# Optimization experiments

Hardware: AMD Instinct MI355X
Metric: run time of the kernel (lower is better)

## Reference

```python
import jax, jax.numpy as jnp
import numpy as np

B = 32; L = 512; D_MODEL = 512; N_LAYERS = 4
D_STATE = 64; D_CONV = 4; EXPAND = 2; HEADDIM = 64; PRED = 96
D_INNER = EXPAND * D_MODEL            # 1024
NHEADS = D_INNER // HEADDIM           # 16
CONV_DIM = D_INNER + 2 * D_STATE      # 1152
D_IN_PROJ = 2 * D_INNER + 2 * D_STATE + NHEADS  # 2192
EPS = 1e-5


def setup_inputs() -> dict:
    key = jax.random.key(0)
    ks = jax.random.split(key, 8)
    s = lambda k, shape, scale=0.02: jax.random.normal(k, shape, jnp.float32) * scale
    return {
        "x": jax.random.normal(ks[0], (B, L, D_MODEL), jnp.float32),
        "in_proj_w": s(ks[1], (N_LAYERS, D_IN_PROJ, D_MODEL)),
        "conv_w": s(ks[2], (N_LAYERS, CONV_DIM, D_CONV), 0.2),
        "conv_b": jnp.zeros((N_LAYERS, CONV_DIM), jnp.float32),
        "dt_bias": jnp.log(jnp.expm1(jax.random.uniform(ks[3], (N_LAYERS, NHEADS), minval=0.001, maxval=0.1))),
        "A_log": jnp.log(jax.random.uniform(ks[4], (N_LAYERS, NHEADS), minval=1.0, maxval=16.0)),
        "Dp": jnp.ones((N_LAYERS, NHEADS), jnp.float32),
        "norm_w": jnp.ones((N_LAYERS, D_INNER), jnp.float32),
        "out_proj_w": s(ks[5], (N_LAYERS, D_MODEL, D_INNER)),
        "ln_w": jnp.ones((N_LAYERS, D_MODEL), jnp.float32),
        "ln_b": jnp.zeros((N_LAYERS, D_MODEL), jnp.float32),
        "final_w": s(ks[6], (D_MODEL, D_MODEL)),
        "final_b": jnp.zeros((D_MODEL,), jnp.float32),
    }


def _silu(x):
    return x * jax.nn.sigmoid(x)


def _causal_dwconv(x, w, b):
    # x: (B, L, C); depthwise causal conv, kernel D_CONV, left pad D_CONV-1
    xt = jnp.swapaxes(x, 1, 2)  # (B, C, L)
    y = jax.lax.conv_general_dilated(
        xt, w[:, None, :], window_strides=(1,), padding=[(D_CONV - 1, 0)],
        feature_group_count=CONV_DIM, dimension_numbers=("NCH", "OIH", "NCH"))
    return jnp.swapaxes(y + b[None, :, None], 1, 2)


def _ssd_scan(xh, dt, Bm, Cm, A, Dp):
    # xh: (B,L,H,P), dt: (B,L,H), Bm/Cm: (B,L,N), A/Dp: (H,)
    dA = jnp.exp(dt * A)  # (B,L,H)

    def step(h, t):
        dA_t, x_t, dt_t, B_t, C_t = t  # (B,H), (B,H,P), (B,H), (B,N), (B,N)
        h = h * dA_t[:, :, None, None] + (dt_t[:, :, None] * x_t)[..., None] * B_t[:, None, None, :]
        y = jnp.einsum("bhpn,bn->bhp", h, C_t)
        return h, y

    Bb, Ll, H, P = xh.shape
    N = Bm.shape[-1]
    h0 = jnp.zeros((Bb, H, P, N), xh.dtype)
    xs = (jnp.moveaxis(dA, 1, 0), jnp.moveaxis(xh, 1, 0), jnp.moveaxis(dt, 1, 0),
          jnp.moveaxis(Bm, 1, 0), jnp.moveaxis(Cm, 1, 0))
    _, ys = jax.lax.scan(step, h0, xs)
    y = jnp.moveaxis(ys, 0, 1)  # (B,L,H,P)
    return y + xh * Dp[None, None, :, None]


def _mamba2(x, w_in, cw, cb, dtb, a_log, dp, nw, w_out):
    zxbcdt = jnp.einsum("bld,ed->ble", x, w_in)  # (B,L,D_IN_PROJ)
    z = zxbcdt[..., :D_INNER]
    xBC = zxbcdt[..., D_INNER:D_INNER + CONV_DIM]
    dt = jax.nn.softplus(zxbcdt[..., -NHEADS:] + dtb)
    xBC = _silu(_causal_dwconv(xBC, cw, cb))
    xh = xBC[..., :D_INNER].reshape(x.shape[0], x.shape[1], NHEADS, HEADDIM)
    Bm = xBC[..., D_INNER:D_INNER + D_STATE]
    Cm = xBC[..., D_INNER + D_STATE:]
    A = -jnp.exp(a_log)
    y = _ssd_scan(xh, dt, Bm, Cm, A, dp).reshape(x.shape[0], x.shape[1], D_INNER)
    # gated RMSNorm (norm_before_gate=False): gate first, then normalize
    y = y * _silu(z)
    y = y * jax.lax.rsqrt(jnp.mean(y * y, axis=-1, keepdims=True) + EPS) * nw
    return jnp.einsum("ble,de->bld", y, w_out)


def _layernorm(x, w, b):
    xc = x - jnp.mean(x, axis=-1, keepdims=True)
    return xc * jax.lax.rsqrt(jnp.mean(xc * xc, axis=-1, keepdims=True) + EPS) * w + b


def reference(x, in_proj_w, conv_w, conv_b, dt_bias, A_log, Dp, norm_w,
              out_proj_w, ln_w, ln_b, final_w, final_b):
    h = x
    for i in range(N_LAYERS):
        res = h
        h = _mamba2(h, in_proj_w[i], conv_w[i], conv_b[i], dt_bias[i],
                    A_log[i], Dp[i], norm_w[i], out_proj_w[i])
        h = _layernorm(h + res, ln_w[i], ln_b[i])
        # dropout is identity in eval mode
    h = h[:, -PRED:, :]
    return jnp.einsum("bld,ed->ble", h, final_w) + final_b
```

## Files before the change

kernel.cpp:

```cpp
#include <hip/hip_runtime.h>
#include <stdint.h>

#define BATCH 32
#define SEQ   512
#define DM    512
#define NL    4
#define DSTATE 64
#define DI    1024
#define NH    16
#define HD    64
#define PREDN 96
#define CDIM  1152
#define CSEG  144
#define DPROJ 2192
#define XBW   1168
#define NC    8
#define EPSF  1e-5f

typedef float  f32x4  __attribute__((ext_vector_type(4)));
typedef __bf16 bf16x4 __attribute__((ext_vector_type(4)));
typedef __bf16 bf16x8 __attribute__((ext_vector_type(8)));

__device__ __forceinline__ float sigmoidf_(float x){ return 1.f/(1.f+__expf(-x)); }
__device__ __forceinline__ float siluf_(float x){ return x*sigmoidf_(x); }
__device__ __forceinline__ float softplusf_(float x){ return (x>20.f)?x:log1pf(__expf(x)); }

__device__ __forceinline__ void gld16(const void* g, void* l){
  __builtin_amdgcn_global_load_lds((__attribute__((address_space(1))) void*)g,
                                   (__attribute__((address_space(3))) void*)l, 16, 0, 0);
}

template<typename TC>
__global__ __launch_bounds__(256) void gemm128(
    const __bf16* __restrict__ A, const __bf16* __restrict__ W,
    TC* __restrict__ C, TC* __restrict__ C2, const float* __restrict__ bias,
    int M, int Nreal, int ldc, int ldc2, int splitN, int K, int remapA)
{
  __shared__ __bf16 sAB[2*128*64];
  __bf16* sA = sAB;
  __bf16* sW = sAB + 128*64;
  const int tid  = threadIdx.x;
  const int m0   = blockIdx.y*128, n0 = blockIdx.x*128;
  const int lane = tid&63, wave = tid>>6;
  const int l15  = lane&15, quad = lane>>4;
  const int wr   = (wave>>1)*64, wc = (wave&1)*64;
  f32x4 acc[4][4];
  #pragma unroll
  for (int a=0;a<4;++a)
    #pragma unroll
    for (int b=0;b<4;++b) acc[a][b] = (f32x4){0,0,0,0};

  for (int k0=0; k0<K; k0+=64){
    #pragma unroll
    for (int j=0;j<4;++j){
      const int f = j*256 + tid;
      const int r = f>>3;
      const int kc = (((f&7) ^ (r&7)))*8;
      int ga = m0 + r;
      if (remapA){ int bb = ga/PREDN; ga = bb*SEQ + (SEQ-PREDN) + (ga - bb*PREDN); }
      gld16(A + (size_t)ga*K + k0 + kc, &sA[f*8]);
      int rb = n0 + r; rb = rb < Nreal ? rb : (Nreal-1);
      gld16(W + (size_t)rb*K + k0 + kc, &sW[f*8]);
    }
    __syncthreads();
    #pragma unroll
    for (int kk=0; kk<64; kk+=32){
      const int kcb = (kk>>3) + quad;
      bf16x8 av[4], bv[4];
      #pragma unroll
      for (int mi=0;mi<4;++mi){
        const int row = wr+mi*16+l15;
        av[mi] = *(const bf16x8*)&sA[row*64 + ((kcb ^ (row&7))<<3)];
      }
      #pragma unroll
      for (int ni=0;ni<4;++ni){
        const int row = wc+ni*16+l15;
        bv[ni] = *(const bf16x8*)&sW[row*64 + ((kcb ^ (row&7))<<3)];
      }
      #pragma unroll
      for (int mi=0;mi<4;++mi)
        #pragma unroll
        for (int ni=0;ni<4;++ni)
          acc[mi][ni] = __builtin_amdgcn_mfma_f32_16x16x32_bf16(av[mi],bv[ni],acc[mi][ni],0,0,0);
    }
    __syncthreads();
  }

  if constexpr (sizeof(TC)==2){
    #pragma unroll
    for (int mi=0;mi<4;++mi)
      #pragma unroll
      for (int ni=0;ni<4;++ni)
        #pragma unroll
        for (int r4=0;r4<4;++r4){
          const int row = wr+mi*16+quad*4+r4;
          const int col = wc+ni*16+l15;
          const int g2  = (col>>3) ^ (row&15);
          sAB[row*128 + g2*8 + (col&7)] = (__bf16)acc[mi][ni][r4];
        }
    __syncthreads();
    #pragma unroll
    for (int it=0; it<8; ++it){
      const int idx = it*256 + tid;
      const int row = idx>>4, g = idx&15;
      const int g2 = g ^ (row&15);
      bf16x8 v = *(const bf16x8*)&sAB[row*128 + g2*8];
      const int col0 = n0 + g*8;
      if (col0 < Nreal){
        const int grow = m0 + row;
        if (col0 < splitN) *(bf16x8*)&C [(size_t)grow*ldc  + col0]          = v;
        else               *(bf16x8*)&C2[(size_t)grow*ldc2 + (col0-splitN)] = v;
      }
    }
  } else {
    #pragma unroll
    for (int ni=0;ni<4;++ni){
      const int col = n0 + wc + ni*16 + l15;
      if (col < Nreal){
        const float badd = bias ? bias[col] : 0.f;
        #pragma unroll
        for (int mi=0;mi<4;++mi){
          #pragma unroll
          for (int r4=0;r4<4;++r4){
            const int row = m0 + wr + mi*16 + quad*4 + r4;
            C[(size_t)row*ldc + col] = (TC)(acc[mi][ni][r4] + badd);
          }
        }
      }
    }
  }
}

__global__ __launch_bounds__(256) void cast4_k(
    const float* __restrict__ s0, __bf16* __restrict__ d0, int n0,
    const float* __restrict__ s1, __bf16* __restrict__ d1, int n1,
    const float* __restrict__ s2, __bf16* __restrict__ d2, int n2,
    const float* __restrict__ s3, __bf16* __restrict__ d3, int n3)
{
  int i = blockIdx.x*256 + threadIdx.x;
  const float* s; __bf16* d;
  if (i < n0){ s=s0; d=d0; }
  else if ((i-=n0) < n1){ s=s1; d=d1; }
  else if ((i-=n1) < n2){ s=s2; d=d2; }
  else if ((i-=n2) < n3){ s=s3; d=d3; }
  else return;
  float4 v = ((const float4*)s)[i];
  bf16x4 o;
  o[0]=(__bf16)v.x; o[1]=(__bf16)v.y; o[2]=(__bf16)v.z; o[3]=(__bf16)v.w;
  ((bf16x4*)d)[i] = o;
}

__global__ __launch_bounds__(256) void conv_silu_k(
    const __bf16* __restrict__ xbw, const float* __restrict__ cw,
    const float* __restrict__ cb, __bf16* __restrict__ xout,
    __bf16* __restrict__ bcout)
{
  int idx = blockIdx.x*256 + threadIdx.x;
  if (idx >= BATCH*SEQ*CSEG) return;
  const int seg = idx % CSEG;
  const int bt  = idx / CSEG;
  const int t = bt % SEQ, b = bt / SEQ;
  const int d0 = seg*8;
  const __bf16* src = xbw + ((size_t)b*SEQ + t)*XBW + d0;
  bf16x8 z8;
  #pragma unroll
  for (int e=0;e<8;++e) z8[e]=(__bf16)0.f;
  bf16x8 x3 = *(const bf16x8*)src;
  bf16x8 x2 = (t>=1)? *(const bf16x8*)(src -   XBW) : z8;
  bf16x8 x1 = (t>=2)? *(const bf16x8*)(src - 2*XBW) : z8;
  bf16x8 x0 = (t>=3)? *(const bf16x8*)(src - 3*XBW) : z8;
  const float4* w4  = (const float4*)(cw + (size_t)d0*4);
  const float4* cb4 = (const float4*)(cb + d0);
  float4 cbl = cb4[0], cbh = cb4[1];
  bf16x8 o;
  #pragma unroll
  for (int e=0;e<8;++e){
    float4 w = w4[e];
    float acc = (e<4 ? (&cbl.x)[e] : (&cbh.x)[e-4])
              + w.x*(float)x0[e] + w.y*(float)x1[e]
              + w.z*(float)x2[e] + w.w*(float)x3[e];
    o[e] = (__bf16)siluf_(acc);
  }
  if (d0 < DI) *(bf16x8*)(xout  + ((size_t)b*SEQ+t)*DI  + d0)       = o;
  else         *(bf16x8*)(bcout + ((size_t)b*SEQ+t)*128 + (d0-DI))  = o;
}

__global__ __launch_bounds__(256) void ssd_fused_k(
    const __bf16* __restrict__ bc,
    __bf16* __restrict__ xy,
    const __bf16* __restrict__ xbw,
    const float* __restrict__ dtb_, const float* __restrict__ alog_,
    const float* __restrict__ dp_)
{
  __shared__ __bf16 sB[64*72], sC[64*72], sXT[64*72], sBwT[64*72],
                    sS[64*72], sHT[64*72];
  __shared__ float sCS[SEQ], sDT[SEQ];
  const int bid = blockIdx.x;
  const int h = bid & 15, b = bid >> 4;
  const int tid = threadIdx.x, wave = tid>>6, lane = tid&63;
  const int l15 = lane&15, quad = lane>>4;
  const int wm = (wave>>1)*32, wn = (wave&1)*32;

  const float Ah  = -__expf(alog_[h]);
  const float dtb = dtb_[h];
  const float Dh  = dp_[h];

  for (int t = tid; t < SEQ; t += 256){
    float raw = (float)xbw[((size_t)b*SEQ + t)*XBW + CDIM + h];
    float dt = softplusf_(raw + dtb);
    sDT[t] = dt;
    sCS[t] = dt*Ah;
  }
  __syncthreads();
  for (int ch = wave; ch < NC; ch += 4){
    float s = sCS[ch*64 + lane];
    #pragma unroll
    for (int off=1; off<64; off<<=1){
      float v = __shfl_up(s, off);
      if (lane >= off) s += v;
    }
    sCS[ch*64 + lane] = s;
  }
  __syncthreads();

  f32x4 run[2][2];
  #pragma unroll
  for (int a=0;a<2;++a)
    #pragma unroll
    for (int d=0;d<2;++d) run[a][d] = (f32x4){0,0,0,0};

  for (int c = 0; c < NC; ++c){
    const int t0 = c*64;
    {
      const int r = tid>>2, seg = (tid&3)*16;
      const __bf16* row = bc + ((size_t)b*SEQ + t0 + r)*128;
      bf16x8 vb0 = *(const bf16x8*)(row + seg);
      bf16x8 vb1 = *(const bf16x8*)(row + seg + 8);
      bf16x8 vc0 = *(const bf16x8*)(row + 64 + seg);
      bf16x8 vc1 = *(const bf16x8*)(row + 64 + seg + 8);
      *(bf16x8*)&sB[r*72+seg]   = vb0;
      *(bf16x8*)&sB[r*72+seg+8] = vb1;
      *(bf16x8*)&sC[r*72+seg]   = vc0;
      *(bf16x8*)&sC[r*72+seg+8] = vc1;
      const float w = __expf(sCS[t0+63] - sCS[t0+r]) * sDT[t0+r];
      #pragma unroll
      for (int e=0;e<8;++e){
        sBwT[(seg+e)*72 + r]   = (__bf16)(w*(float)vb0[e]);
        sBwT[(seg+8+e)*72 + r] = (__bf16)(w*(float)vb1[e]);
      }
      const __bf16* xrow = xy + ((size_t)b*SEQ + t0 + r)*DI + h*64;
      bf16x8 vx0 = *(const bf16x8*)(xrow + seg);
      bf16x8 vx1 = *(const bf16x8*)(xrow + seg + 8);
      #pragma unroll
      for (int e=0;e<8;++e){
        sXT[(seg+e)*72 + r]   = vx0[e];
        sXT[(seg+8+e)*72 + r] = vx1[e];
      }
    }
    __syncthreads();

    f32x4 aS[2][2];
    #pragma unroll
    for (int a=0;a<2;++a)
      #pragma unroll
      for (int d=0;d<2;++d) aS[a][d] = (f32x4){0,0,0,0};
    #pragma unroll
    for (int kk=0; kk<64; kk+=32){
      const int kf = kk + quad*8;
      bf16x8 a0 = *(const bf16x8*)&sC[(wm+l15)*72+kf];
      bf16x8 a1 = *(const bf16x8*)&sC[(wm+16+l15)*72+kf];
      bf16x8 b0 = *(const bf16x8*)&sB[(wn+l15)*72+kf];
      bf16x8 b1 = *(const bf16x8*)&sB[(wn+16+l15)*72+kf];
      aS[0][0] = __builtin_amdgcn_mfma_f32_16x16x32_bf16(a0,b0,aS[0][0],0,0,0);
      aS[0][1] = __builtin_amdgcn_mfma_f32_16x16x32_bf16(a0,b1,aS[0][1],0,0,0);
      aS[1][0] = __builtin_amdgcn_mfma_f32_16x16x32_bf16(a1,b0,aS[1][0],0,0,0);
      aS[1][1] = __builtin_amdgcn_mfma_f32_16x16x32_bf16(a1,b1,aS[1][1],0,0,0);
    }
    #pragma unroll
    for (int mi=0;mi<2;++mi)
      #pragma unroll
      for (int ni=0;ni<2;++ni)
        #pragma unroll
        for (int r4=0;r4<4;++r4){
          const int i = wm+mi*16+quad*4+r4, j = wn+ni*16+l15;
          float ed = __expf(fminf(sCS[t0+i]-sCS[t0+j], 0.f)) * sDT[t0+j];
          float v = aS[mi][ni][r4]*ed;
          sS[i*72+j] = (__bf16)((j<=i)? v : 0.f);
          sHT[j*72+i] = (__bf16)run[mi][ni][r4];
        }
    __syncthreads();

    f32x4 aY[2][2], aH[2][2], aYi[2][2];
    #pragma unroll
    for (int a=0;a<2;++a)
      #pragma unroll
      for (int d=0;d<2;++d){
        aY[a][d]=(f32x4){0,0,0,0}; aH[a][d]=(f32x4){0,0,0,0};
        aYi[a][d]=(f32x4){0,0,0,0};
      }
    #pragma unroll
    for (int kk=0; kk<64; kk+=32){
      const int kf = kk + quad*8;
      bf16x8 b0 = *(const bf16x8*)&sXT[(wn+l15)*72+kf];
      bf16x8 b1 = *(const bf16x8*)&sXT[(wn+16+l15)*72+kf];
      bf16x8 s0 = *(const bf16x8*)&sS[(wm+l15)*72+kf];
      bf16x8 s1 = *(const bf16x8*)&sS[(wm+16+l15)*72+kf];
      bf16x8 w0 = *(const bf16x8*)&sBwT[(wm+l15)*72+kf];
      bf16x8 w1 = *(const bf16x8*)&sBwT[(wm+16+l15)*72+kf];
      bf16x8 c0 = *(const bf16x8*)&sC[(wm+l15)*72+kf];
      bf16x8 c1 = *(const bf16x8*)&sC[(wm+16+l15)*72+kf];
      bf16x8 h0 = *(const bf16x8*)&sHT[(wn+l15)*72+kf];
      bf16x8 h1 = *(const bf16x8*)&sHT[(wn+16+l15)*72+kf];
      aY[0][0] = __builtin_amdgcn_mfma_f32_16x16x32_bf16(s0,b0,aY[0][0],0,0,0);
      aY[0][1] = __builtin_amdgcn_mfma_f32_16x16x32_bf16(s0,b1,aY[0][1],0,0,0);
      aY[1][0] = __builtin_amdgcn_mfma_f32_16x16x32_bf16(s1,b0,aY[1][0],0,0,0);
      aY[1][1] = __builtin_amdgcn_mfma_f32_16x16x32_bf16(s1,b1,aY[1][1],0,0,0);
      aH[0][0] = __builtin_amdgcn_mfma_f32_16x16x32_bf16(w0,b0,aH[0][0],0,0,0);
      aH[0][1] = __builtin_amdgcn_mfma_f32_16x16x32_bf16(w0,b1,aH[0][1],0,0,0);
      aH[1][0] = __builtin_amdgcn_mfma_f32_16x16x32_bf16(w1,b0,aH[1][0],0,0,0);
      aH[1][1] = __builtin_amdgcn_mfma_f32_16x16x32_bf16(w1,b1,aH[1][1],0,0,0);
      aYi[0][0] = __builtin_amdgcn_mfma_f32_16x16x32_bf16(c0,h0,aYi[0][0],0,0,0);
      aYi[0][1] = __builtin_amdgcn_mfma_f32_16x16x32_bf16(c0,h1,aYi[0][1],0,0,0);
      aYi[1][0] = __builtin_amdgcn_mfma_f32_16x16x32_bf16(c1,h0,aYi[1][0],0,0,0);
      aYi[1][1] = __builtin_amdgcn_mfma_f32_16x16x32_bf16(c1,h1,aYi[1][1],0,0,0);
    }

    const float lam = __expf(sCS[t0+63]);
    #pragma unroll
    for (int mi=0;mi<2;++mi)
      #pragma unroll
      for (int ni=0;ni<2;++ni)
        #pragma unroll
        for (int r4=0;r4<4;++r4){
          const int i = wm+mi*16+quad*4+r4;
          const int p = wn+ni*16+l15;
          const float xval = (float)sXT[p*72 + i];
          const float e2 = __expf(sCS[t0+i]);
          const float yv = aY[mi][ni][r4] + Dh*xval + e2*aYi[mi][ni][r4];
          xy[((size_t)b*SEQ + t0 + i)*DI + h*64 + p] = (__bf16)yv;
          run[mi][ni][r4] = run[mi][ni][r4]*lam + aH[mi][ni][r4];
        }
    __syncthreads();
  }
}

__global__ __launch_bounds__(256) void gate_rms_k(
    __bf16* __restrict__ y, const __bf16* __restrict__ z, const float* __restrict__ nw)
{
  __shared__ float red[4];
  const int tid = threadIdx.x;
  const int sub = tid>>7;
  const int off = (tid&127)*8;
  const size_t row = (size_t)blockIdx.x*2 + sub;
  __bf16* yrow = y + row*DI;
  const __bf16* zrow = z + row*DI;
  bf16x8 yv = *(const bf16x8*)(yrow+off);
  bf16x8 zv = *(const bf16x8*)(zrow+off);
  float u[8]; float ss = 0.f;
  #pragma unroll
  for (int e=0;e<8;++e){
    float uu = (float)yv[e]*siluf_((float)zv[e]);
    u[e]=uu; ss += uu*uu;
  }
  #pragma unroll
  for (int o=32;o;o>>=1) ss += __shfl_xor(ss,o);
  if ((tid&63)==0) red[tid>>6] = ss;
  __syncthreads();
  ss = red[sub*2] + red[sub*2+1];
  const float sc = rsqrtf(ss*(1.f/DI) + EPSF);
  const float4* nw4 = (const float4*)(nw + off);
  float4 n0 = nw4[0], n1 = nw4[1];
  bf16x8 o;
  #pragma unroll
  for (int e=0;e<8;++e)
    o[e] = (__bf16)(u[e]*sc*(e<4 ? (&n0.x)[e] : (&n1.x)[e-4]));
  *(bf16x8*)(yrow+off) = o;
}

__global__ __launch_bounds__(256) void add_ln_k(
    const __bf16* __restrict__ tmp, __bf16* __restrict__ resio,
    const float* __restrict__ w, const float* __restrict__ bb)
{
  const int tid = threadIdx.x, lane = tid&63;
  const size_t row = (size_t)blockIdx.x*4 + (tid>>6);
  const int off = lane*8;
  const __bf16* trow = tmp + row*DM;
  __bf16* rrow = resio + row*DM;
  bf16x8 tv = *(const bf16x8*)(trow+off);
  bf16x8 rv = *(const bf16x8*)(rrow+off);
  float v[8]; float s = 0.f;
  #pragma unroll
  for (int e=0;e<8;++e){ v[e]=(float)tv[e]+(float)rv[e]; s += v[e]; }
  #pragma unroll
  for (int o=32;o;o>>=1) s += __shfl_xor(s,o);
  const float mean = s*(1.f/DM);
  float q = 0.f;
  #pragma unroll
  for (int e=0;e<8;++e){ v[e]-=mean; q += v[e]*v[e]; }
  #pragma unroll
  for (int o=32;o;o>>=1) q += __shfl_xor(q,o);
  const float rstd = rsqrtf(q*(1.f/DM) + EPSF);
  const float4* w4 = (const float4*)(w + off);
  const float4* b4 = (const float4*)(bb + off);
  float4 w0=w4[0], w1=w4[1], b0=b4[0], b1=b4[1];
  bf16x8 o8;
  #pragma unroll
  for (int e=0;e<8;++e){
    float we = e<4 ? (&w0.x)[e] : (&w1.x)[e-4];
    float be = e<4 ? (&b0.x)[e] : (&b1.x)[e-4];
    o8[e] = (__bf16)(v[e]*rstd*we + be);
  }
  *(bf16x8*)(rrow+off) = o8;
}

extern "C" void kernel_launch(void* const* d_in, const int* in_sizes, int n_in,
                              void* d_out, int out_size, void* d_ws, size_t ws_size,
                              hipStream_t stream)
{
  const float* x         = (const float*)d_in[0];
  const float* in_proj_w = (const float*)d_in[1];
  const float* conv_w    = (const float*)d_in[2];
  const float* conv_b    = (const float*)d_in[3];
  const float* dt_bias   = (const float*)d_in[4];
  const float* A_log     = (const float*)d_in[5];
  const float* Dp        = (const float*)d_in[6];
  const float* norm_w    = (const float*)d_in[7];
  const float* out_proj_w= (const float*)d_in[8];
  const float* ln_w      = (const float*)d_in[9];
  const float* ln_b      = (const float*)d_in[10];
  const float* final_w   = (const float*)d_in[11];
  const float* final_b   = (const float*)d_in[12];
  float* out = (float*)d_out;

  const size_t ROWS = (size_t)BATCH*SEQ;
  __bf16* wbf_in  = (__bf16*)d_ws;
  __bf16* wbf_out = wbf_in  + (size_t)NL*DPROJ*DM;
  __bf16* wbf_fin = wbf_out + (size_t)NL*DM*DI;
  __bf16* zbuf    = wbf_fin + (size_t)DM*DM;
  __bf16* xbw     = zbuf    + ROWS*DI;
  __bf16* ybuf    = xbw     + ROWS*XBW;
  __bf16* bcb     = ybuf    + ROWS*DI;
  __bf16* xcur    = bcb     + ROWS*128;
  __bf16* tmp  = xbw;

  {
    int n1 = NL*DPROJ*DM/4, n2 = NL*DM*DI/4, n3 = DM*DM/4, n4 = (int)(ROWS*DM/4);
    int tot = n1+n2+n3+n4;
    cast4_k<<<(tot+255)/256, 256, 0, stream>>>(
        in_proj_w, wbf_in, n1, out_proj_w, wbf_out, n2,
        final_w, wbf_fin, n3, x, xcur, n4);
  }

  const int convTotal = BATCH*SEQ*CSEG;
  const int BIGN = 1<<30;

  for (int l=0; l<NL; ++l){
    const __bf16* wl = wbf_in + (size_t)l*DPROJ*DM;
    gemm128<__bf16><<<dim3((DPROJ+127)/128, (int)(ROWS/128)), 256, 0, stream>>>(
        xcur, wl, zbuf, xbw, nullptr, (int)ROWS, DPROJ, DI, XBW, DI, DM, 0);
    conv_silu_k<<<(convTotal+255)/256, 256, 0, stream>>>(
        xbw, conv_w + (size_t)l*CDIM*4, conv_b + (size_t)l*CDIM, ybuf, bcb);
    ssd_fused_k<<<BATCH*NH, 256, 0, stream>>>(
        bcb, ybuf, xbw, dt_bias + l*NH, A_log + l*NH, Dp + l*NH);
    gate_rms_k<<<(int)(ROWS/2), 256, 0, stream>>>(ybuf, zbuf, norm_w + (size_t)l*DI);
    gemm128<__bf16><<<dim3(DM/128, (int)(ROWS/128)), 256, 0, stream>>>(
        ybuf, wbf_out + (size_t)l*DM*DI, tmp, tmp, nullptr, (int)ROWS, DM, DM, DM, BIGN, DI, 0);
    add_ln_k<<<(int)(ROWS/4), 256, 0, stream>>>(tmp, xcur, ln_w + l*DM, ln_b + l*DM);
  }
  gemm128<float><<<dim3(DM/128, (BATCH*PREDN)/128), 256, 0, stream>>>(
      xcur, wbf_fin, out, out, final_b, BATCH*PREDN, DM, DM, DM, BIGN, DM, 1);
}
```

Measured before the change: 866.0 us.

## Add 64-row GEMM tile, swap grid axes, and prefetch next SSD chunk

Adds a gemm64 kernel with a 64x128 tile for the out-projection and final projection, giving more blocks on the small-N GEMMs so more compute units are busy. The gemm128 grid is transposed so consecutive blocks share a weight column tile instead of an activation row tile, which changes L2 reuse. The SSD kernel now loads the next chunk's B, C and x into registers while the current chunk is computed, hiding global load latency at the cost of extra registers.

```diff
diff --git a/kernel.cpp b/kernel.cpp
--- a/kernel.cpp
+++ b/kernel.cpp
@@ -40,7 +40,7 @@
   __bf16* sA = sAB;
   __bf16* sW = sAB + 128*64;
   const int tid  = threadIdx.x;
-  const int m0   = blockIdx.y*128, n0 = blockIdx.x*128;
+  const int m0   = blockIdx.x*128, n0 = blockIdx.y*128;
   const int lane = tid&63, wave = tid>>6;
   const int l15  = lane&15, quad = lane>>4;
   const int wr   = (wave>>1)*64, wc = (wave&1)*64;
@@ -120,6 +120,110 @@
         const float badd = bias ? bias[col] : 0.f;
         #pragma unroll
         for (int mi=0;mi<4;++mi){
+          #pragma unroll
+          for (int r4=0;r4<4;++r4){
+            const int row = m0 + wr + mi*16 + quad*4 + r4;
+            C[(size_t)row*ldc + col] = (TC)(acc[mi][ni][r4] + badd);
+          }
+        }
+      }
+    }
+  }
+}
+
+template<typename TC>
+__global__ __launch_bounds__(256) void gemm64(
+    const __bf16* __restrict__ A, const __bf16* __restrict__ W,
+    TC* __restrict__ C, const float* __restrict__ bias,
+    int M, int Nreal, int ldc, int K, int remapA)
+{
+  __shared__ __bf16 sPool[64*64 + 128*64];
+  __bf16* sA = sPool;
+  __bf16* sW = sPool + 64*64;
+  const int tid  = threadIdx.x;
+  const int m0   = blockIdx.x*64, n0 = blockIdx.y*128;
+  const int lane = tid&63, wave = tid>>6;
+  const int l15  = lane&15, quad = lane>>4;
+  const int wr   = (wave&1)*32, wc = (wave>>1)*64;
+  f32x4 acc[2][4];
+  #pragma unroll
+  for (int a=0;a<2;++a)
+    #pragma unroll
+    for (int b=0;b<4;++b) acc[a][b] = (f32x4){0,0,0,0};
+
+  for (int k0=0; k0<K; k0+=64){
+    #pragma unroll
+    for (int j=0;j<2;++j){
+      const int f = j*256 + tid;
+      const int r = f>>3;
+      const int kc = (((f&7) ^ (r&7)))*8;
+      int ga = m0 + r;
+      if (remapA){ int bb = ga/PREDN; ga = bb*SEQ + (SEQ-PREDN) + (ga - bb*PREDN); }
+      gld16(A + (size_t)ga*K + k0 + kc, &sA[f*8]);
+    }
+    #pragma unroll
+    for (int j=0;j<4;++j){
+      const int f = j*256 + tid;
+      const int r = f>>3;
+      const int kc = (((f&7) ^ (r&7)))*8;
+      int rb = n0 + r; rb = rb < Nreal ? rb : (Nreal-1);
+      gld16(W + (size_t)rb*K + k0 + kc, &sW[f*8]);
+    }
+    __syncthreads();
+    #pragma unroll
+    for (int kk=0; kk<64; kk+=32){
+      const int kcb = (kk>>3) + quad;
+      bf16x8 av[2], bv[4];
+      #pragma unroll
+      for (int mi=0;mi<2;++mi){
+        const int row = wr+mi*16+l15;
+        av[mi] = *(const bf16x8*)&sA[row*64 + ((kcb ^ (row&7))<<3)];
+      }
+      #pragma unroll
+      for (int ni=0;ni<4;++ni){
+        const int row = wc+ni*16+l15;
+        bv[ni] = *(const bf16x8*)&sW[row*64 + ((kcb ^ (row&7))<<3)];
+      }
+      #pragma unroll
+      for (int mi=0;mi<2;++mi)
+        #pragma unroll
+        for (int ni=0;ni<4;++ni)
+          acc[mi][ni] = __builtin_amdgcn_mfma_f32_16x16x32_bf16(av[mi],bv[ni],acc[mi][ni],0,0,0);
+    }
+    __syncthreads();
+  }
+
+  if constexpr (sizeof(TC)==2){
+    #pragma unroll
+    for (int mi=0;mi<2;++mi)
+      #pragma unroll
+      for (int ni=0;ni<4;++ni)
+        #pragma unroll
+        for (int r4=0;r4<4;++r4){
+          const int row = wr+mi*16+quad*4+r4;
+          const int col = wc+ni*16+l15;
+          const int g2  = (col>>3) ^ (row&15);
+          sPool[row*128 + g2*8 + (col&7)] = (__bf16)acc[mi][ni][r4];
+        }
+    __syncthreads();
+    #pragma unroll
+    for (int it=0; it<4; ++it){
+      const int idx = it*256 + tid;
+      const int row = idx>>4, g = idx&15;
+      const int g2 = g ^ (row&15);
+      bf16x8 v = *(const bf16x8*)&sPool[row*128 + g2*8];
+      const int col0 = n0 + g*8;
+      if (col0 < Nreal)
+        *(bf16x8*)&C[(size_t)(m0+row)*ldc + col0] = v;
+    }
+  } else {
+    #pragma unroll
+    for (int ni=0;ni<4;++ni){
+      const int col = n0 + wc + ni*16 + l15;
+      if (col < Nreal){
+        const float badd = bias ? bias[col] : 0.f;
+        #pragma unroll
+        for (int mi=0;mi<2;++mi){
           #pragma unroll
           for (int r4=0;r4<4;++r4){
             const int row = m0 + wr + mi*16 + quad*4 + r4;
@@ -229,35 +333,46 @@
     #pragma unroll
     for (int d=0;d<2;++d) run[a][d] = (f32x4){0,0,0,0};
 
+  const int r = tid>>2, seg = (tid&3)*16;
+  bf16x8 pb0, pb1, pc0, pc1, px0, px1;
+  {
+    const __bf16* row = bc + ((size_t)b*SEQ + r)*128;
+    pb0 = *(const bf16x8*)(row + seg);
+    pb1 = *(const bf16x8*)(row + seg + 8);
+    pc0 = *(const bf16x8*)(row + 64 + seg);
+    pc1 = *(const bf16x8*)(row + 64 + seg + 8);
+    const __bf16* xrow = xy + ((size_t)b*SEQ + r)*DI + h*64;
+    px0 = *(const bf16x8*)(xrow + seg);
+    px1 = *(const bf16x8*)(xrow + seg + 8);
+  }
+
   for (int c = 0; c < NC; ++c){
     const int t0 = c*64;
     {
-      const int r = tid>>2, seg = (tid&3)*16;
-      const __bf16* row = bc + ((size_t)b*SEQ + t0 + r)*128;
-      bf16x8 vb0 = *(const bf16x8*)(row + seg);
-      bf16x8 vb1 = *(const bf16x8*)(row + seg + 8);
-      bf16x8 vc0 = *(const bf16x8*)(row + 64 + seg);
-      bf16x8 vc1 = *(const bf16x8*)(row + 64 + seg + 8);
-      *(bf16x8*)&sB[r*72+seg]   = vb0;
-      *(bf16x8*)&sB[r*72+seg+8] = vb1;
-      *(bf16x8*)&sC[r*72+seg]   = vc0;
-      *(bf16x8*)&sC[r*72+seg+8] = vc1;
+      *(bf16x8*)&sB[r*72+seg]   = pb0;
+      *(bf16x8*)&sB[r*72+seg+8] = pb1;
+      *(bf16x8*)&sC[r*72+seg]   = pc0;
+      *(bf16x8*)&sC[r*72+seg+8] = pc1;
       const float w = __expf(sCS[t0+63] - sCS[t0+r]) * sDT[t0+r];
       #pragma unroll
       for (int e=0;e<8;++e){
-        sBwT[(seg+e)*72 + r]   = (__bf16)(w*(float)vb0[e]);
-        sBwT[(seg+8+e)*72 + r] = (__bf16)(w*(float)vb1[e]);
-      }
-      const __bf16* xrow = xy + ((size_t)b*SEQ + t0 + r)*DI + h*64;
-      bf16x8 vx0 = *(const bf16x8*)(xrow + seg);
-      bf16x8 vx1 = *(const bf16x8*)(xrow + seg + 8);
-      #pragma unroll
-      for (int e=0;e<8;++e){
-        sXT[(seg+e)*72 + r]   = vx0[e];
-        sXT[(seg+8+e)*72 + r] = vx1[e];
-      }
-    }
-    __syncthreads();
+        sBwT[(seg+e)*72 + r]   = (__bf16)(w*(float)pb0[e]);
+        sBwT[(seg+8+e)*72 + r] = (__bf16)(w*(float)pb1[e]);
+        sXT[(seg+e)*72 + r]    = px0[e];
+        sXT[(seg+8+e)*72 + r]  = px1[e];
+      }
+    }
+    __syncthreads();
+    if (c+1 < NC){
+      const __bf16* row = bc + ((size_t)b*SEQ + t0 + 64 + r)*128;
+      pb0 = *(const bf16x8*)(row + seg);
+      pb1 = *(const bf16x8*)(row + seg + 8);
+      pc0 = *(const bf16x8*)(row + 64 + seg);
+      pc1 = *(const bf16x8*)(row + 64 + seg + 8);
+      const __bf16* xrow = xy + ((size_t)b*SEQ + t0 + 64 + r)*DI + h*64;
+      px0 = *(const bf16x8*)(xrow + seg);
+      px1 = *(const bf16x8*)(xrow + seg + 8);
+    }
 
     f32x4 aS[2][2];
     #pragma unroll
@@ -452,21 +567,20 @@
   }
 
   const int convTotal = BATCH*SEQ*CSEG;
-  const int BIGN = 1<<30;
 
   for (int l=0; l<NL; ++l){
     const __bf16* wl = wbf_in + (size_t)l*DPROJ*DM;
-    gemm128<__bf16><<<dim3((DPROJ+127)/128, (int)(ROWS/128)), 256, 0, stream>>>(
+    gemm128<__bf16><<<dim3((int)(ROWS/128), (DPROJ+127)/128), 256, 0, stream>>>(
         xcur, wl, zbuf, xbw, nullptr, (int)ROWS, DPROJ, DI, XBW, DI, DM, 0);
     conv_silu_k<<<(convTotal+255)/256, 256, 0, stream>>>(
         xbw, conv_w + (size_t)l*CDIM*4, conv_b + (size_t)l*CDIM, ybuf, bcb);
     ssd_fused_k<<<BATCH*NH, 256, 0, stream>>>(
         bcb, ybuf, xbw, dt_bias + l*NH, A_log + l*NH, Dp + l*NH);
     gate_rms_k<<<(int)(ROWS/2), 256, 0, stream>>>(ybuf, zbuf, norm_w + (size_t)l*DI);
-    gemm128<__bf16><<<dim3(DM/128, (int)(ROWS/128)), 256, 0, stream>>>(
-        ybuf, wbf_out + (size_t)l*DM*DI, tmp, tmp, nullptr, (int)ROWS, DM, DM, DM, BIGN, DI, 0);
+    gemm64<__bf16><<<dim3((int)(ROWS/64), DM/128), 256, 0, stream>>>(
+        ybuf, wbf_out + (size_t)l*DM*DI, tmp, nullptr, (int)ROWS, DM, DM, DI, 0);
     add_ln_k<<<(int)(ROWS/4), 256, 0, stream>>>(tmp, xcur, ln_w + l*DM, ln_b + l*DM);
   }
-  gemm128<float><<<dim3(DM/128, (BATCH*PREDN)/128), 256, 0, stream>>>(
-      xcur, wbf_fin, out, out, final_b, BATCH*PREDN, DM, DM, DM, BIGN, DM, 1);
-}
+  gemm64<float><<<dim3((BATCH*PREDN)/64, DM/128), 256, 0, stream>>>(
+      xcur, wbf_fin, out, final_b, BATCH*PREDN, DM, DM, DM, 1);
+}
```

After: 857.9 us. Within noise of the previous version (-0.9%).
